# Performance work log

Hardware: AMD Instinct MI355X
Metric: run time of the kernel (lower is better)

Reference implementation:

```python
import jax, jax.numpy as jnp
import numpy as np
from jax import lax

CHANNELS = 32

def _sobel_kernels(channels):
    kx = np.array([[[1,0,-1],[2,0,-2],[1,0,-1]],
                   [[2,0,-2],[4,0,-4],[2,0,-2]],
                   [[1,0,-1],[2,0,-2],[1,0,-1]]], dtype=np.float32)
    ky = np.array([[[1,2,1],[0,0,0],[-1,-2,-1]],
                   [[2,4,2],[0,0,0],[-2,-4,-2]],
                   [[1,2,1],[0,0,0],[-1,-2,-1]]], dtype=np.float32)
    kz = np.array([[[1,2,1],[2,4,2],[1,2,1]],
                   [[0,0,0],[0,0,0],[0,0,0]],
                   [[-1,-2,-1],[-2,-4,-2],[-1,-2,-1]]], dtype=np.float32)
    # depthwise kernels: (C, 1, 3, 3, 3) in OIDHW with feature_group_count=C
    rep = lambda k: jnp.asarray(np.broadcast_to(k[None, None], (channels, 1, 3, 3, 3)).copy())
    return rep(kx), rep(ky), rep(kz)

def setup_inputs() -> dict:
    key = jax.random.key(0)
    x = jax.random.normal(key, (2, CHANNELS, 64, 128, 128), dtype=jnp.float32)
    kx, ky, kz = _sobel_kernels(CHANNELS)
    return {"x": x, "kernel_x": kx, "kernel_y": ky, "kernel_z": kz}

def _dwconv3d(x, k):
    # depthwise 3x3x3 conv, stride 1, padding 1 (SAME for odd kernel)
    return lax.conv_general_dilated(
        x, k,
        window_strides=(1, 1, 1),
        padding=((1, 1), (1, 1), (1, 1)),
        dimension_numbers=("NCDHW", "OIDHW", "NCDHW"),
        feature_group_count=x.shape[1],
    )

def reference(x, kernel_x, kernel_y, kernel_z):
    gx = _dwconv3d(x, kernel_x)
    gy = _dwconv3d(x, kernel_y)
    gz = _dwconv3d(x, kernel_z)
    return jnp.sqrt(gx * gx + gy * gy + gz * gz + 1e-6)
```

## Files before the change

kernel.cpp:

```cpp
#include <hip/hip_runtime.h>


typedef float floatx4 __attribute__((ext_vector_type(4)));

constexpr int W   = 128;
constexpr int H   = 128;
constexpr int DZ  = 64;
constexpr int NC  = 2 * 32;
constexpr int TH  = 8;
constexpr int HBLKS = H / TH;
constexpr int ZCH = 2;
constexpr int ZLEN = DZ / ZCH;

__global__ __launch_bounds__(256, 6)
void sobel3d_kernel(const float* __restrict__ xg, float* __restrict__ og) {
    const int tid = threadIdx.x;
    const int tx  = tid & 31;
    const int ty  = tid >> 5;
    int b = blockIdx.x;
    const int hblk = b % HBLKS; b /= HBLKS;
    const int zc   = b % ZCH;   b /= ZCH;
    const int nc   = b;
    const int h    = hblk * TH + ty;
    const int za   = zc * ZLEN;
    const int zb   = za + ZLEN;
    const int lastv = (zb < DZ) ? zb : DZ - 1;

    const size_t HW = (size_t)H * W;
    const float* __restrict__ xp = xg + (size_t)nc * DZ * HW;
    float* __restrict__ op       = og + (size_t)nc * DZ * HW;

    const bool hm = (h > 0);
    const bool hp = (h < H - 1);
    const size_t roff = (size_t)h * W + 4 * tx;

    auto load3 = [&](const float* p, floatx4& a, floatx4& bq, floatx4& c) {
        a  = hm ? *(const floatx4*)(p - W) : (floatx4){0.f, 0.f, 0.f, 0.f};
        bq = *(const floatx4*)p;
        c  = hp ? *(const floatx4*)(p + W) : (floatx4){0.f, 0.f, 0.f, 0.f};
    };

    auto plane_sde = [&](floatx4 qA, floatx4 qB, floatx4 qC,
                         floatx4& cc, floatx4& dd, floatx4& ee) {
        floatx4 u = qA + 2.f * qB + qC;
        floatx4 v = qA - qC;
        float um1 = __shfl_up(u.w, 1, 64);   if (tx == 0)  um1 = 0.f;
        float up4 = __shfl_down(u.x, 1, 64); if (tx == 31) up4 = 0.f;
        float vm1 = __shfl_up(v.w, 1, 64);   if (tx == 0)  vm1 = 0.f;
        float vp4 = __shfl_down(v.x, 1, 64); if (tx == 31) vp4 = 0.f;
        cc.x = um1 + 2.f * u.x + u.y;
        cc.y = u.x + 2.f * u.y + u.z;
        cc.z = u.y + 2.f * u.z + u.w;
        cc.w = u.z + 2.f * u.w + up4;
        ee.x = um1 - u.y;
        ee.y = u.x - u.z;
        ee.z = u.y - u.w;
        ee.w = u.z - up4;
        dd.x = vm1 + 2.f * v.x + v.y;
        dd.y = v.x + 2.f * v.y + v.z;
        dd.z = v.y + 2.f * v.z + v.w;
        dd.w = v.z + 2.f * v.w + vp4;
    };

    floatx4 cP, dP, eP, cC, dCv, eC;
    const float* pin = xp + (size_t)za * HW + roff;
    {
        floatx4 a, bq, c;
        if (za > 0) { load3(pin - HW, a, bq, c); plane_sde(a, bq, c, cP, dP, eP); }
        else        { cP = dP = eP = (floatx4){0.f, 0.f, 0.f, 0.f}; }
        load3(pin, a, bq, c); plane_sde(a, bq, c, cC, dCv, eC);
    }
    floatx4 pA, pB, pC;
    load3(pin + HW, pA, pB, pC);
    pin += 2 * HW;
    float* pout = op + (size_t)za * HW + roff;

#pragma unroll 2
    for (int z = za; z < zb; ++z) {
        floatx4 nA, nB, nC;
        if (z + 2 <= lastv) load3(pin, nA, nB, nC);
        else { nA = nB = nC = (floatx4){0.f, 0.f, 0.f, 0.f}; }
        pin += HW;

        floatx4 c2, d2, e2;
        plane_sde(pA, pB, pC, c2, d2, e2);

        floatx4 gx = eP + 2.f * eC + e2;
        floatx4 gy = dP + 2.f * dCv + d2;
        floatx4 gz = cP - c2;
        floatx4 o;
        o.x = __builtin_amdgcn_sqrtf(gx.x * gx.x + gy.x * gy.x + gz.x * gz.x + 1e-6f);
        o.y = __builtin_amdgcn_sqrtf(gx.y * gx.y + gy.y * gy.y + gz.y * gz.y + 1e-6f);
        o.z = __builtin_amdgcn_sqrtf(gx.z * gx.z + gy.z * gy.z + gz.z * gz.z + 1e-6f);
        o.w = __builtin_amdgcn_sqrtf(gx.w * gx.w + gy.w * gy.w + gz.w * gz.w + 1e-6f);
        __builtin_nontemporal_store(o, (floatx4*)pout);
        pout += HW;

        cP = cC;  cC  = c2;
        dP = dCv; dCv = d2;
        eP = eC;  eC  = e2;
        pA = nA;  pB  = nB;  pC = nC;
    }
}

extern "C" void kernel_launch(void* const* d_in, const int* in_sizes, int n_in,
                              void* d_out, int out_size, void* d_ws, size_t ws_size,
                              hipStream_t stream) {
    const float* x = (const float*)d_in[0];
    float* out = (float*)d_out;
    dim3 grid(NC * ZCH * HBLKS);
    dim3 block(256);
    sobel3d_kernel<<<grid, block, 0, stream>>>(x, out);
}
```

Measured before the change: 96.53 us.

## Share middle rows across half-waves via shuffle and deepen the plane prefetch

Each thread now loads two rows per plane (its own row and one outer neighbour) instead of three. The other neighbour row comes from the partner half-wave through __shfl_xor by 32, which holds the adjacent row in the 64-lane wavefront. The z-loop also prefetches two planes ahead instead of one, to hide more load latency. This cuts redundant global and L2 load traffic but adds four cross-lane shuffles per plane and more live registers. The kernel is likely already near DRAM bandwidth, so the benefit may be limited.

```diff
diff --git a/kernel.cpp b/kernel.cpp
--- a/kernel.cpp
+++ b/kernel.cpp
@@ -30,20 +30,25 @@
     const float* __restrict__ xp = xg + (size_t)nc * DZ * HW;
     float* __restrict__ op       = og + (size_t)nc * DZ * HW;
 
-    const bool hm = (h > 0);
-    const bool hp = (h < H - 1);
-    const size_t roff = (size_t)h * W + 4 * tx;
+    const int  h_out  = h + ((ty & 1) ? 1 : -1);
+    const bool ovalid = ((unsigned)h_out < (unsigned)H);
+    const size_t roff  = (size_t)h * W + 4 * tx;
+    const int    wdelta = ((ty & 1) ? W : -W);
 
-    auto load3 = [&](const float* p, floatx4& a, floatx4& bq, floatx4& c) {
-        a  = hm ? *(const floatx4*)(p - W) : (floatx4){0.f, 0.f, 0.f, 0.f};
-        bq = *(const floatx4*)p;
-        c  = hp ? *(const floatx4*)(p + W) : (floatx4){0.f, 0.f, 0.f, 0.f};
+    auto loadpair = [&](const float* p, floatx4& mid, floatx4& out) {
+        mid = *(const floatx4*)p;
+        out = ovalid ? *(const floatx4*)(p + wdelta) : (floatx4){0.f, 0.f, 0.f, 0.f};
     };
 
-    auto plane_sde = [&](floatx4 qA, floatx4 qB, floatx4 qC,
+    auto plane_sde = [&](floatx4 mid, floatx4 out,
                          floatx4& cc, floatx4& dd, floatx4& ee) {
-        floatx4 u = qA + 2.f * qB + qC;
-        floatx4 v = qA - qC;
+        floatx4 inn;
+        inn.x = __shfl_xor(mid.x, 32, 64);
+        inn.y = __shfl_xor(mid.y, 32, 64);
+        inn.z = __shfl_xor(mid.z, 32, 64);
+        inn.w = __shfl_xor(mid.w, 32, 64);
+        floatx4 u = out + 2.f * mid + inn;
+        floatx4 v = out - inn;
         float um1 = __shfl_up(u.w, 1, 64);   if (tx == 0)  um1 = 0.f;
         float up4 = __shfl_down(u.x, 1, 64); if (tx == 31) up4 = 0.f;
         float vm1 = __shfl_up(v.w, 1, 64);   if (tx == 0)  vm1 = 0.f;
@@ -65,25 +70,26 @@
     floatx4 cP, dP, eP, cC, dCv, eC;
     const float* pin = xp + (size_t)za * HW + roff;
     {
-        floatx4 a, bq, c;
-        if (za > 0) { load3(pin - HW, a, bq, c); plane_sde(a, bq, c, cP, dP, eP); }
+        floatx4 m, o;
+        if (za > 0) { loadpair(pin - HW, m, o); plane_sde(m, o, cP, dP, eP); }
         else        { cP = dP = eP = (floatx4){0.f, 0.f, 0.f, 0.f}; }
-        load3(pin, a, bq, c); plane_sde(a, bq, c, cC, dCv, eC);
+        loadpair(pin, m, o); plane_sde(m, o, cC, dCv, eC);
     }
-    floatx4 pA, pB, pC;
-    load3(pin + HW, pA, pB, pC);
-    pin += 2 * HW;
+    floatx4 pM, pO, qM, qO;
+    loadpair(pin + HW,     pM, pO);
+    loadpair(pin + 2 * HW, qM, qO);
+    pin += 3 * HW;
     float* pout = op + (size_t)za * HW + roff;
 
 #pragma unroll 2
     for (int z = za; z < zb; ++z) {
-        floatx4 nA, nB, nC;
-        if (z + 2 <= lastv) load3(pin, nA, nB, nC);
-        else { nA = nB = nC = (floatx4){0.f, 0.f, 0.f, 0.f}; }
+        floatx4 nM, nO;
+        if (z + 3 <= lastv) loadpair(pin, nM, nO);
+        else { nM = nO = (floatx4){0.f, 0.f, 0.f, 0.f}; }
         pin += HW;
 
         floatx4 c2, d2, e2;
-        plane_sde(pA, pB, pC, c2, d2, e2);
+        plane_sde(pM, pO, c2, d2, e2);
 
         floatx4 gx = eP + 2.f * eC + e2;
         floatx4 gy = dP + 2.f * dCv + d2;
@@ -99,7 +105,8 @@
         cP = cC;  cC  = c2;
         dP = dCv; dCv = d2;
         eP = eC;  eC  = e2;
-        pA = nA;  pB  = nB;  pC = nC;
+        pM = qM;  pO  = qO;
+        qM = nM;  qO  = nO;
     }
 }
 
```

After: 100.3 us. 1.04x slower.
